# Kernel optimization log

Hardware: AMD Instinct MI355X
Metric: run time of the kernel (lower is better)

## Reference

```python
import jax, jax.numpy as jnp
import numpy as np

B, S, D, H, DFF = 4, 2048, 1024, 16, 4096
DK = D // H
EPS = 1e-5


def setup_inputs() -> dict:
    key = jax.random.key(0)
    ks = jax.random.split(key, 10)
    s = 0.02
    return {
        "x": jax.random.normal(ks[0], (B, S, D), jnp.float32),
        "wq": jax.random.normal(ks[1], (D, D), jnp.float32) * s,
        "wk": jax.random.normal(ks[2], (D, D), jnp.float32) * s,
        "wv": jax.random.normal(ks[3], (D, D), jnp.float32) * s,
        "wo": jax.random.normal(ks[4], (D, D), jnp.float32) * s,
        "w1": jax.random.normal(ks[5], (D, DFF), jnp.float32) * s,
        "b1": jnp.zeros((DFF,), jnp.float32),
        "w2": jax.random.normal(ks[6], (DFF, D), jnp.float32) * s,
        "b2": jnp.zeros((D,), jnp.float32),
        "g1": jnp.ones((D,), jnp.float32),
        "be1": jnp.zeros((D,), jnp.float32),
        "g2": jnp.ones((D,), jnp.float32),
        "be2": jnp.zeros((D,), jnp.float32),
    }


def _layernorm(x, g, b):
    mu = jnp.mean(x, axis=-1, keepdims=True)
    var = jnp.mean(jnp.square(x - mu), axis=-1, keepdims=True)
    return (x - mu) * jax.lax.rsqrt(var + EPS) * g + b


def reference(x, wq, wk, wv, wo, w1, b1, w2, b2, g1, be1, g2, be2):
    # --- self-attention block (pre-LN) ---
    residual = x
    h = _layernorm(x, g1, be1)
    q = (h @ wq).reshape(B, S, H, DK).transpose(0, 2, 1, 3)  # [B,H,S,DK]
    k = (h @ wk).reshape(B, S, H, DK).transpose(0, 2, 1, 3)
    v = (h @ wv).reshape(B, S, H, DK).transpose(0, 2, 1, 3)
    scores = jnp.einsum("bhqd,bhkd->bhqk", q, k) / jnp.sqrt(jnp.float32(DK))
    weights = jax.nn.softmax(scores, axis=-1)
    weights = jnp.nan_to_num(weights, nan=0.0)
    attn = jnp.einsum("bhqk,bhkd->bhqd", weights, v)
    attn = attn.transpose(0, 2, 1, 3).reshape(B, S, D)
    x = residual + attn @ wo
    # --- FFN block (pre-LN) ---
    residual = x
    h = _layernorm(x, g2, be2)
    h = jax.nn.relu(h @ w1 + b1) @ w2 + b2
    return residual + h
```

## Files before the change

kernel.cpp:

```cpp
#include <hip/hip_runtime.h>
#include <stdint.h>

#define B_ 4
#define S_ 2048
#define D_ 1024
#define H_ 16
#define DFF_ 4096
#define QSTR 3072

typedef __attribute__((ext_vector_type(8))) short short8;
typedef __attribute__((ext_vector_type(4))) short short4v;
typedef __attribute__((ext_vector_type(4))) float floatx4;
typedef __attribute__((ext_vector_type(16))) float floatx16;

typedef const __attribute__((address_space(1))) void* gas_ptr;
typedef __attribute__((address_space(3))) void* las_ptr;

__device__ __forceinline__ short f2bf(float f) {
  union { float f; uint32_t u; } v; v.f = f;
  uint32_t r = v.u + 0x7fffu + ((v.u >> 16) & 1u);
  return (short)(r >> 16);
}

__global__ __launch_bounds__(256) void ln_kernel(
    const float* __restrict__ x, const float* __restrict__ g,
    const float* __restrict__ be, short* __restrict__ out)
{
  const int row = blockIdx.x;
  const int tid = threadIdx.x;
  const float4 v = ((const float4*)(x + (size_t)row * D_))[tid];
  float s1 = v.x + v.y + v.z + v.w;
  float s2 = v.x*v.x + v.y*v.y + v.z*v.z + v.w*v.w;
#pragma unroll
  for (int off = 1; off < 64; off <<= 1) {
    s1 += __shfl_xor(s1, off);
    s2 += __shfl_xor(s2, off);
  }
  __shared__ float r1[4], r2[4];
  if ((tid & 63) == 0) { r1[tid >> 6] = s1; r2[tid >> 6] = s2; }
  __syncthreads();
  s1 = r1[0] + r1[1] + r1[2] + r1[3];
  s2 = r2[0] + r2[1] + r2[2] + r2[3];
  const float mu = s1 * (1.0f / D_);
  const float var = s2 * (1.0f / D_) - mu * mu;
  const float rs = rsqrtf(var + 1e-5f);
  const float4 gv = ((const float4*)g)[tid];
  const float4 bv = ((const float4*)be)[tid];
  short4v o;
  o.x = f2bf((v.x - mu) * rs * gv.x + bv.x);
  o.y = f2bf((v.y - mu) * rs * gv.y + bv.y);
  o.z = f2bf((v.z - mu) * rs * gv.z + bv.z);
  o.w = f2bf((v.w - mu) * rs * gv.w + bv.w);
  *(short4v*)&out[(size_t)row * D_ + tid * 4] = o;
}

__global__ __launch_bounds__(256) void transpose_all(
    const float* __restrict__ wq, const float* __restrict__ wk,
    const float* __restrict__ wv, const float* __restrict__ wo,
    const float* __restrict__ w1, const float* __restrict__ w2,
    short* __restrict__ wqkvT, short* __restrict__ woT,
    short* __restrict__ w1T, short* __restrict__ w2T)
{
  const uint32_t pid = blockIdx.x;
  const float* in; short* out;
  int R, C, tile, xsh;
  if (pid < 4096) {
    const int which = pid >> 10; tile = pid & 1023;
    R = 1024; C = 1024; xsh = 5;
    in  = (which == 0) ? wq : (which == 1) ? wk : (which == 2) ? wv : wo;
    out = (which == 3) ? woT : wqkvT + (size_t)which * 1024 * 1024;
  } else if (pid < 8192) {
    tile = pid - 4096; R = 1024; C = 4096; xsh = 7; in = w1; out = w1T;
  } else {
    tile = pid - 8192; R = 4096; C = 1024; xsh = 5; in = w2; out = w2T;
  }
  const int c0 = (tile & ((1 << xsh) - 1)) * 32;
  const int r0 = (tile >> xsh) * 32;

  __shared__ float t[32][33];
  const int tx = threadIdx.x & 31, ty = threadIdx.x >> 5;
#pragma unroll
  for (int i = 0; i < 4; i++)
    t[ty + i * 8][tx] = in[(size_t)(r0 + ty + i * 8) * C + c0 + tx];
  __syncthreads();
#pragma unroll
  for (int i = 0; i < 4; i++)
    out[(size_t)(c0 + ty + i * 8) * R + r0 + tx] = f2bf(t[tx][ty + i * 8]);
}

__global__ __launch_bounds__(256, 4) void gemm_bt(
    const short* __restrict__ A, const short* __restrict__ Bt,
    float* __restrict__ outf, short* __restrict__ outb,
    short* __restrict__ outbK, short* __restrict__ vtT,
    const float* __restrict__ bias, const float* __restrict__ resid,
    int M, int N, int K, int do_relu, int split, int group)
{
  __shared__ short As[2 * 128 * 32];
  __shared__ short Bs[2 * 128 * 32];
  const int tid = threadIdx.x;
  const int wave = tid >> 6;
  const int lane = tid & 63;
  const int quad = lane >> 4;
  const int l16 = lane & 15;

  const uint32_t nblk = gridDim.x;
  const uint32_t pid = blockIdx.y * nblk + blockIdx.x;
  const uint32_t nig = (uint32_t)group * nblk;
  const uint32_t gid = pid / nig;
  const uint32_t within = pid - gid * nig;
  const uint32_t bm = gid * group + within % group;
  const uint32_t bn = within / group;
  const int tm = bm * 128;
  const int tn = bn * 128;

  const int wm = (wave & 1) * 64;
  const int wn = (wave >> 1) * 64;
  const int srow = lane >> 2;
  const int scol = ((lane & 3) ^ ((lane >> 3) & 3)) * 8;
  const int rg = (l16 >> 1) & 3;

  floatx4 acc[4][4];
#pragma unroll
  for (int i = 0; i < 4; i++)
#pragma unroll
    for (int j = 0; j < 4; j++) acc[i][j] = floatx4{0.f, 0.f, 0.f, 0.f};

  const short* gA0 = A + (size_t)(tm + wave * 32 + srow) * K + scol;
  const short* gB0 = Bt + (size_t)(tn + wave * 32 + srow) * K + scol;

  for (int kt = 0; kt < K; kt += 64) {
    __syncthreads();
    __builtin_amdgcn_global_load_lds((gas_ptr)(gA0 + kt),                      (las_ptr)(&As[wave * 1024]),        16, 0, 0);
    __builtin_amdgcn_global_load_lds((gas_ptr)(gA0 + kt + (size_t)16 * K),     (las_ptr)(&As[wave * 1024 + 512]),  16, 0, 0);
    __builtin_amdgcn_global_load_lds((gas_ptr)(gB0 + kt),                      (las_ptr)(&Bs[wave * 1024]),        16, 0, 0);
    __builtin_amdgcn_global_load_lds((gas_ptr)(gB0 + kt + (size_t)16 * K),     (las_ptr)(&Bs[wave * 1024 + 512]),  16, 0, 0);
    __builtin_amdgcn_global_load_lds((gas_ptr)(gA0 + kt + 32),                 (las_ptr)(&As[4096 + wave * 1024]),       16, 0, 0);
    __builtin_amdgcn_global_load_lds((gas_ptr)(gA0 + kt + 32 + (size_t)16 * K),(las_ptr)(&As[4096 + wave * 1024 + 512]), 16, 0, 0);
    __builtin_amdgcn_global_load_lds((gas_ptr)(gB0 + kt + 32),                 (las_ptr)(&Bs[4096 + wave * 1024]),       16, 0, 0);
    __builtin_amdgcn_global_load_lds((gas_ptr)(gB0 + kt + 32 + (size_t)16 * K),(las_ptr)(&Bs[4096 + wave * 1024 + 512]), 16, 0, 0);
    __syncthreads();

#pragma unroll
    for (int ksub = 0; ksub < 2; ksub++) {
      const int hb = ksub * 4096;
      short8 af[4], bfv[4];
#pragma unroll
      for (int mi = 0; mi < 4; mi++)
        af[mi] = *(const short8*)&As[hb + (wm + mi * 16 + l16) * 32 + (quad ^ rg) * 8];
#pragma unroll
      for (int ni = 0; ni < 4; ni++)
        bfv[ni] = *(const short8*)&Bs[hb + (wn + ni * 16 + l16) * 32 + (quad ^ rg) * 8];
#pragma unroll
      for (int mi = 0; mi < 4; mi++)
#pragma unroll
        for (int ni = 0; ni < 4; ni++)
          acc[mi][ni] = __builtin_amdgcn_mfma_f32_16x16x32_bf16(af[mi], bfv[ni], acc[mi][ni], 0, 0, 0);
    }
  }

  short* ob = outb;
  int Nst = N;
  int cbase = tn;
  int vpart = 0;
  if (split) {
    const int part = tn >> 10;
    if (part == 2) vpart = 1;
    else ob = (part == 0) ? outb : outbK;
    Nst = D_;
    cbase = tn & (D_ - 1);
  }

  if (vpart) {
#pragma unroll
    for (int mi = 0; mi < 4; mi++) {
      const int row0 = tm + wm + mi * 16 + quad * 4;
      const int bb = row0 >> 11, s0r = row0 & 2047;
#pragma unroll
      for (int ni = 0; ni < 4; ni++) {
        const int cst = cbase + wn + ni * 16 + l16;
        short4v o;
#pragma unroll
        for (int r = 0; r < 4; r++) o[r] = f2bf(acc[mi][ni][r]);
        *(short4v*)&vtT[((size_t)(bb << 10) + cst) * (size_t)S_ + s0r] = o;
      }
    }
    return;
  }

#pragma unroll
  for (int mi = 0; mi < 4; mi++) {
    const int row0 = tm + wm + mi * 16 + quad * 4;
#pragma unroll
    for (int ni = 0; ni < 4; ni++) {
      const int col = tn + wn + ni * 16 + l16;
      const int cst = cbase + wn + ni * 16 + l16;
      const float bv = bias ? bias[col] : 0.0f;
#pragma unroll
      for (int r = 0; r < 4; r++) {
        const size_t idx = (size_t)(row0 + r) * Nst + cst;
        float v = acc[mi][ni][r] + bv;
        if (do_relu) v = fmaxf(v, 0.0f);
        if (resid) v += resid[idx];
        if (outf) outf[idx] = v;
        if (ob) ob[idx] = f2bf(v);
      }
    }
  }
}

__global__ __launch_bounds__(256, 4) void gemm_bt_n64(
    const short* __restrict__ A, const short* __restrict__ Bt,
    float* __restrict__ outf,
    const float* __restrict__ bias, const float* __restrict__ resid,
    int M, int N, int K, int group)
{
  __shared__ short As[2 * 128 * 32];
  __shared__ short Bs[2 * 64 * 32];
  const int tid = threadIdx.x;
  const int wave = tid >> 6;
  const int lane = tid & 63;
  const int quad = lane >> 4;
  const int l16 = lane & 15;

  const uint32_t nblk = gridDim.x;
  const uint32_t pid = blockIdx.y * nblk + blockIdx.x;
  const uint32_t nig = (uint32_t)group * nblk;
  const uint32_t gid = pid / nig;
  const uint32_t within = pid - gid * nig;
  const uint32_t bm = gid * group + within % group;
  const uint32_t bn = within / group;
  const int tm = bm * 128;
  const int tn = bn * 64;

  const int wm = (wave & 1) * 64;
  const int wn = (wave >> 1) * 32;
  const int srow = lane >> 2;
  const int scol = (lane & 3) * 8;

  floatx4 acc[4][2];
#pragma unroll
  for (int i = 0; i < 4; i++)
#pragma unroll
    for (int j = 0; j < 2; j++) acc[i][j] = floatx4{0.f, 0.f, 0.f, 0.f};

  const short* gA0 = A + (size_t)(tm + wave * 32 + srow) * K + scol;
  const short* gB0 = Bt + (size_t)(tn + wave * 16 + srow) * K + scol;

  for (int kt = 0; kt < K; kt += 64) {
    __syncthreads();
    __builtin_amdgcn_global_load_lds((gas_ptr)(gA0 + kt),                      (las_ptr)(&As[wave * 1024]),        16, 0, 0);
    __builtin_amdgcn_global_load_lds((gas_ptr)(gA0 + kt + (size_t)16 * K),     (las_ptr)(&As[wave * 1024 + 512]),  16, 0, 0);
    __builtin_amdgcn_global_load_lds((gas_ptr)(gA0 + kt + 32),                 (las_ptr)(&As[4096 + wave * 1024]),       16, 0, 0);
    __builtin_amdgcn_global_load_lds((gas_ptr)(gA0 + kt + 32 + (size_t)16 * K),(las_ptr)(&As[4096 + wave * 1024 + 512]), 16, 0, 0);
    __builtin_amdgcn_global_load_lds((gas_ptr)(gB0 + kt),      (las_ptr)(&Bs[wave * 512]),        16, 0, 0);
    __builtin_amdgcn_global_load_lds((gas_ptr)(gB0 + kt + 32), (las_ptr)(&Bs[2048 + wave * 512]), 16, 0, 0);
    __syncthreads();

#pragma unroll
    for (int ksub = 0; ksub < 2; ksub++) {
      const int ha = ksub * 4096;
      const int hbv = ksub * 2048;
      short8 af[4], bfv[2];
#pragma unroll
      for (int mi = 0; mi < 4; mi++)
        af[mi] = *(const short8*)&As[ha + (wm + mi * 16 + l16) * 32 + quad * 8];
#pragma unroll
      for (int ni = 0; ni < 2; ni++)
        bfv[ni] = *(const short8*)&Bs[hbv + (wn + ni * 16 + l16) * 32 + quad * 8];
#pragma unroll
      for (int mi = 0; mi < 4; mi++)
#pragma unroll
        for (int ni = 0; ni < 2; ni++)
          acc[mi][ni] = __builtin_amdgcn_mfma_f32_16x16x32_bf16(af[mi], bfv[ni], acc[mi][ni], 0, 0, 0);
    }
  }

#pragma unroll
  for (int mi = 0; mi < 4; mi++) {
    const int row0 = tm + wm + mi * 16 + quad * 4;
#pragma unroll
    for (int ni = 0; ni < 2; ni++) {
      const int col = tn + wn + ni * 16 + l16;
      const float bv = bias ? bias[col] : 0.0f;
#pragma unroll
      for (int r = 0; r < 4; r++) {
        const size_t idx = (size_t)(row0 + r) * N + col;
        float v = acc[mi][ni][r] + bv;
        if (resid) v += resid[idx];
        outf[idx] = v;
      }
    }
  }
}

__device__ __forceinline__ int swz64(int row) {
  return (row & 7) ^ ((row >> 3) & 3);
}
__device__ __forceinline__ int kvidx(int row, int scol) {
  return (row << 6) + (scol ^ (swz64(row) << 3));
}

__global__ __launch_bounds__(256, 4) void attn_kernel(
    const short* __restrict__ qb, const short* __restrict__ kb,
    const short* __restrict__ vtb, short* __restrict__ attb)
{
  __shared__ short Ks[2][64 * 64];
  __shared__ short Vts[2][64 * 64];
  __shared__ float lbuf[4][32];

  const int tid = threadIdx.x;
  const int wave = tid >> 6, lane = tid & 63;
  const int l31 = lane & 31, hi = lane >> 5;
  const int qt = blockIdx.x, bh = blockIdx.y;
  const int b = bh >> 4, h = bh & 15;
  const size_t rowbase = (size_t)b * S_;
  const int hcol = h * 64;

  const int lr = lane >> 3, lg = lane & 7;
  const int sgran = (lg ^ lr ^ wave) * 8;
  const short* ksrc = kb + (rowbase + wave * 8 + lr) * D_ + hcol + sgran;
  const short* vsrc = vtb + ((size_t)bh * 64 + wave * 8 + lr) * S_ + sgran;

  short8 qf[4];
  {
    const short* gq = qb + (rowbase + qt * 128 + wave * 32 + l31) * D_ + hcol + hi * 8;
#pragma unroll
    for (int st = 0; st < 4; st++) {
      short8 t = *(const short8*)(gq + st * 16);
#pragma unroll
      for (int i = 0; i < 8; i++) {
        const float f = __uint_as_float(((uint32_t)(uint16_t)t[i]) << 16) * 0.18033688f;
        t[i] = (short)((__float_as_uint(f) + 0x8000u) >> 16);
      }
      qf[st] = t;
    }
  }

  floatx16 Of[2];
#pragma unroll
  for (int nd = 0; nd < 2; nd++)
#pragma unroll
    for (int i = 0; i < 16; i++) Of[nd][i] = 0.f;
  float lrun0 = 0.f, lrun1 = 0.f;

  __builtin_amdgcn_global_load_lds((gas_ptr)ksrc,                      (las_ptr)(&Ks[0][(wave * 8) * 64]),        16, 0, 0);
  __builtin_amdgcn_global_load_lds((gas_ptr)(ksrc + (size_t)32 * D_),  (las_ptr)(&Ks[0][(32 + wave * 8) * 64]),   16, 0, 0);
  __builtin_amdgcn_global_load_lds((gas_ptr)vsrc,                      (las_ptr)(&Vts[0][(wave * 8) * 64]),       16, 0, 0);
  __builtin_amdgcn_global_load_lds((gas_ptr)(vsrc + (size_t)32 * S_),  (las_ptr)(&Vts[0][(32 + wave * 8) * 64]),  16, 0, 0);

  for (int kt = 0; kt < S_; kt += 64) {
    const int cur = (kt >> 6) & 1;
    __syncthreads();

    if (kt + 64 < S_) {
      const int nxt = cur ^ 1;
      const short* kp = ksrc + (size_t)(kt + 64) * D_;
      const short* vp = vsrc + (kt + 64);
      __builtin_amdgcn_global_load_lds((gas_ptr)kp,                      (las_ptr)(&Ks[nxt][(wave * 8) * 64]),        16, 0, 0);
      __builtin_amdgcn_global_load_lds((gas_ptr)(kp + (size_t)32 * D_),  (las_ptr)(&Ks[nxt][(32 + wave * 8) * 64]),   16, 0, 0);
      __builtin_amdgcn_global_load_lds((gas_ptr)vp,                      (las_ptr)(&Vts[nxt][(wave * 8) * 64]),       16, 0, 0);
      __builtin_amdgcn_global_load_lds((gas_ptr)(vp + (size_t)32 * S_),  (las_ptr)(&Vts[nxt][(32 + wave * 8) * 64]),  16, 0, 0);
    }

#pragma unroll
    for (int sub = 0; sub < 2; sub++) {
      floatx16 s;
#pragma unroll
      for (int i = 0; i < 16; i++) s[i] = 0.f;
      __builtin_amdgcn_s_setprio(1);
#pragma unroll
      for (int st = 0; st < 4; st++) {
        const short8 kf = *(const short8*)&Ks[cur][kvidx(sub * 32 + l31, st * 16 + hi * 8)];
        s = __builtin_amdgcn_mfma_f32_32x32x16_bf16(kf, qf[st], s, 0, 0, 0);
      }
      __builtin_amdgcn_s_setprio(0);
      float p[16];
#pragma unroll
      for (int i = 0; i < 16; i++) {
        p[i] = __builtin_amdgcn_exp2f(s[i]);
        if (i & 1) lrun1 += p[i]; else lrun0 += p[i];
      }
      short8 pf[2];
#pragma unroll
      for (int kw = 0; kw < 2; kw++) {
        const int o = kw * 8;
        uint32_t wa, wb, wc, wd;
        asm("v_cvt_pk_bf16_f32 %0, %1, %2" : "=v"(wa) : "v"(p[o + 0]), "v"(p[o + 1]));
        asm("v_cvt_pk_bf16_f32 %0, %1, %2" : "=v"(wb) : "v"(p[o + 4]), "v"(p[o + 5]));
        asm("v_cvt_pk_bf16_f32 %0, %1, %2" : "=v"(wc) : "v"(p[o + 2]), "v"(p[o + 3]));
        asm("v_cvt_pk_bf16_f32 %0, %1, %2" : "=v"(wd) : "v"(p[o + 6]), "v"(p[o + 7]));
        asm("v_permlane32_swap_b32 %0, %1" : "+v"(wa), "+v"(wb));
        asm("v_permlane32_swap_b32 %0, %1" : "+v"(wc), "+v"(wd));
        union { uint32_t u[4]; short8 s8; } pk;
        pk.u[0] = wa; pk.u[1] = wc; pk.u[2] = wb; pk.u[3] = wd;
        pf[kw] = pk.s8;
      }
      __builtin_amdgcn_s_setprio(1);
#pragma unroll
      for (int kw = 0; kw < 2; kw++)
#pragma unroll
        for (int nd = 0; nd < 2; nd++) {
          const short8 vf = *(const short8*)&Vts[cur][kvidx(nd * 32 + l31, sub * 32 + kw * 16 + hi * 8)];
          Of[nd] = __builtin_amdgcn_mfma_f32_32x32x16_bf16(pf[kw], vf, Of[nd], 0, 0, 0);
        }
      __builtin_amdgcn_s_setprio(0);
    }
  }

  const float lrun = lrun0 + lrun1;
  const float ltot = lrun + __shfl_xor(lrun, 32);
  if (hi == 0) lbuf[wave][l31] = ltot;
  asm volatile("" ::: "memory");
#pragma unroll
  for (int reg = 0; reg < 16; reg++) {
    const int q = (reg & 3) + 4 * hi + 8 * (reg >> 2);
    const float inv = 1.0f / lbuf[wave][q];
    const size_t base = (rowbase + qt * 128 + wave * 32 + q) * D_ + hcol + l31;
    attb[base]      = f2bf(Of[0][reg] * inv);
    attb[base + 32] = f2bf(Of[1][reg] * inv);
  }
}

extern "C" void kernel_launch(void* const* d_in, const int* in_sizes, int n_in,
                              void* d_out, int out_size, void* d_ws, size_t ws_size,
                              hipStream_t stream) {
  const float* x   = (const float*)d_in[0];
  const float* wq  = (const float*)d_in[1];
  const float* wk  = (const float*)d_in[2];
  const float* wv  = (const float*)d_in[3];
  const float* wo  = (const float*)d_in[4];
  const float* w1  = (const float*)d_in[5];
  const float* b1  = (const float*)d_in[6];
  const float* w2  = (const float*)d_in[7];
  const float* b2  = (const float*)d_in[8];
  const float* g1  = (const float*)d_in[9];
  const float* be1 = (const float*)d_in[10];
  const float* g2  = (const float*)d_in[11];
  const float* be2 = (const float*)d_in[12];
  float* out = (float*)d_out;

  const size_t MROWS = (size_t)B_ * S_;
  char* p = (char*)d_ws;
  auto take = [&](size_t bytes) { char* r = p; p += (bytes + 255) & ~(size_t)255; return r; };
  short* hb    = (short*)take(MROWS * D_ * 2);
  short* h2b   = (short*)take(MROWS * D_ * 2);
  short* qbuf  = (short*)take(MROWS * D_ * 2);
  short* kbuf  = (short*)take(MROWS * D_ * 2);
  short* vtb   = (short*)take(MROWS * D_ * 2);
  short* attb  = (short*)take(MROWS * D_ * 2);
  short* ffb   = (short*)take(MROWS * DFF_ * 2);
  short* wqkvT = (short*)take((size_t)3 * D_ * D_ * 2);
  short* woT   = (short*)take((size_t)D_ * D_ * 2);
  short* w1T   = (short*)take((size_t)D_ * DFF_ * 2);
  short* w2T   = (short*)take((size_t)DFF_ * D_ * 2);
  float* x1    = (float*)take(MROWS * D_ * 4);

  transpose_all<<<12288, 256, 0, stream>>>(wq, wk, wv, wo, w1, w2,
                                           wqkvT, woT, w1T, w2T);

  ln_kernel<<<MROWS, 256, 0, stream>>>(x, g1, be1, hb);

  gemm_bt<<<dim3(QSTR / 128, MROWS / 128), 256, 0, stream>>>(
      hb, wqkvT, nullptr, qbuf, kbuf, vtb, nullptr, nullptr, MROWS, QSTR, D_, 0, 1, 8);

  attn_kernel<<<dim3(S_ / 128, B_ * H_), 256, 0, stream>>>(qbuf, kbuf, vtb, attb);

  gemm_bt<<<dim3(D_ / 128, MROWS / 128), 256, 0, stream>>>(
      attb, woT, x1, nullptr, nullptr, nullptr, nullptr, x, MROWS, D_, D_, 0, 0, 8);

  ln_kernel<<<MROWS, 256, 0, stream>>>(x1, g2, be2, h2b);

  gemm_bt<<<dim3(DFF_ / 128, MROWS / 128), 256, 0, stream>>>(
      h2b, w1T, nullptr, ffb, nullptr, nullptr, b1, nullptr, MROWS, DFF_, D_, 1, 0, 8);

  gemm_bt<<<dim3(D_ / 128, MROWS / 128), 256, 0, stream>>>(
      ffb, w2T, out, nullptr, nullptr, nullptr, b2, x1, MROWS, D_, DFF_, 0, 0, 8);

  (void)in_sizes; (void)n_in; (void)out_size; (void)ws_size;
}
```

Measured before the change: 528.6 us.

## Double-buffer GEMM LDS tiles and prefetch next K-slice during MFMA compute

Restructures the main bf16 GEMM loop into a two-stage ping-pong pipeline. The tile for step k+1 is loaded asynchronously into the alternate LDS buffer while MFMAs run on the current one, with one barrier per 32-wide K step instead of two per 64-wide step. It also raises wave priority around the MFMA block and removes the unused-looking N=64 GEMM variant. This should hide global-to-LDS latency, at the cost of twice as many loop iterations and barriers. The visible code does not show whether the host still calls the removed N=64 kernel.

```diff
diff --git a/kernel.cpp b/kernel.cpp
--- a/kernel.cpp
+++ b/kernel.cpp
@@ -95,8 +95,8 @@
     const float* __restrict__ bias, const float* __restrict__ resid,
     int M, int N, int K, int do_relu, int split, int group)
 {
-  __shared__ short As[2 * 128 * 32];
-  __shared__ short Bs[2 * 128 * 32];
+  __shared__ short As[2][128 * 32];
+  __shared__ short Bs[2][128 * 32];
   const int tid = threadIdx.x;
   const int wave = tid >> 6;
   const int lane = tid & 63;
@@ -116,7 +116,7 @@
   const int wm = (wave & 1) * 64;
   const int wn = (wave >> 1) * 64;
   const int srow = lane >> 2;
-  const int scol = ((lane & 3) ^ ((lane >> 3) & 3)) * 8;
+  const int sgran = ((lane & 3) ^ ((lane >> 3) & 3)) * 8;
   const int rg = (l16 >> 1) & 3;
 
   floatx4 acc[4][4];
@@ -125,38 +125,41 @@
 #pragma unroll
     for (int j = 0; j < 4; j++) acc[i][j] = floatx4{0.f, 0.f, 0.f, 0.f};
 
-  const short* gA0 = A + (size_t)(tm + wave * 32 + srow) * K + scol;
-  const short* gB0 = Bt + (size_t)(tn + wave * 32 + srow) * K + scol;
-
-  for (int kt = 0; kt < K; kt += 64) {
+  const short* gA0 = A + (size_t)(tm + wave * 32 + srow) * K + sgran;
+  const short* gB0 = Bt + (size_t)(tn + wave * 32 + srow) * K + sgran;
+
+#define GB_STAGE(buf, kk)                                                                                   \
+  do {                                                                                                      \
+    __builtin_amdgcn_global_load_lds((gas_ptr)(gA0 + (kk)),                   (las_ptr)(&As[buf][wave * 1024]),       16, 0, 0); \
+    __builtin_amdgcn_global_load_lds((gas_ptr)(gA0 + (kk) + (size_t)16 * K),  (las_ptr)(&As[buf][wave * 1024 + 512]), 16, 0, 0); \
+    __builtin_amdgcn_global_load_lds((gas_ptr)(gB0 + (kk)),                   (las_ptr)(&Bs[buf][wave * 1024]),       16, 0, 0); \
+    __builtin_amdgcn_global_load_lds((gas_ptr)(gB0 + (kk) + (size_t)16 * K),  (las_ptr)(&Bs[buf][wave * 1024 + 512]), 16, 0, 0); \
+  } while (0)
+
+  GB_STAGE(0, 0);
+
+  for (int kt = 0; kt < K; kt += 32) {
+    const int cur = (kt >> 5) & 1;
     __syncthreads();
-    __builtin_amdgcn_global_load_lds((gas_ptr)(gA0 + kt),                      (las_ptr)(&As[wave * 1024]),        16, 0, 0);
-    __builtin_amdgcn_global_load_lds((gas_ptr)(gA0 + kt + (size_t)16 * K),     (las_ptr)(&As[wave * 1024 + 512]),  16, 0, 0);
-    __builtin_amdgcn_global_load_lds((gas_ptr)(gB0 + kt),                      (las_ptr)(&Bs[wave * 1024]),        16, 0, 0);
-    __builtin_amdgcn_global_load_lds((gas_ptr)(gB0 + kt + (size_t)16 * K),     (las_ptr)(&Bs[wave * 1024 + 512]),  16, 0, 0);
-    __builtin_amdgcn_global_load_lds((gas_ptr)(gA0 + kt + 32),                 (las_ptr)(&As[4096 + wave * 1024]),       16, 0, 0);
-    __builtin_amdgcn_global_load_lds((gas_ptr)(gA0 + kt + 32 + (size_t)16 * K),(las_ptr)(&As[4096 + wave * 1024 + 512]), 16, 0, 0);
-    __builtin_amdgcn_global_load_lds((gas_ptr)(gB0 + kt + 32),                 (las_ptr)(&Bs[4096 + wave * 1024]),       16, 0, 0);
-    __builtin_amdgcn_global_load_lds((gas_ptr)(gB0 + kt + 32 + (size_t)16 * K),(las_ptr)(&Bs[4096 + wave * 1024 + 512]), 16, 0, 0);
-    __syncthreads();
-
-#pragma unroll
-    for (int ksub = 0; ksub < 2; ksub++) {
-      const int hb = ksub * 4096;
-      short8 af[4], bfv[4];
-#pragma unroll
-      for (int mi = 0; mi < 4; mi++)
-        af[mi] = *(const short8*)&As[hb + (wm + mi * 16 + l16) * 32 + (quad ^ rg) * 8];
+
+    if (kt + 32 < K) GB_STAGE(cur ^ 1, kt + 32);
+
+    short8 af[4], bfv[4];
+#pragma unroll
+    for (int mi = 0; mi < 4; mi++)
+      af[mi] = *(const short8*)&As[cur][(wm + mi * 16 + l16) * 32 + (quad ^ rg) * 8];
+#pragma unroll
+    for (int ni = 0; ni < 4; ni++)
+      bfv[ni] = *(const short8*)&Bs[cur][(wn + ni * 16 + l16) * 32 + (quad ^ rg) * 8];
+    __builtin_amdgcn_s_setprio(1);
+#pragma unroll
+    for (int mi = 0; mi < 4; mi++)
 #pragma unroll
       for (int ni = 0; ni < 4; ni++)
-        bfv[ni] = *(const short8*)&Bs[hb + (wn + ni * 16 + l16) * 32 + (quad ^ rg) * 8];
-#pragma unroll
-      for (int mi = 0; mi < 4; mi++)
-#pragma unroll
-        for (int ni = 0; ni < 4; ni++)
-          acc[mi][ni] = __builtin_amdgcn_mfma_f32_16x16x32_bf16(af[mi], bfv[ni], acc[mi][ni], 0, 0, 0);
-    }
-  }
+        acc[mi][ni] = __builtin_amdgcn_mfma_f32_16x16x32_bf16(af[mi], bfv[ni], acc[mi][ni], 0, 0, 0);
+    __builtin_amdgcn_s_setprio(0);
+  }
+#undef GB_STAGE
 
   short* ob = outb;
   int Nst = N;
@@ -203,91 +206,6 @@
         if (resid) v += resid[idx];
         if (outf) outf[idx] = v;
         if (ob) ob[idx] = f2bf(v);
-      }
-    }
-  }
-}
-
-__global__ __launch_bounds__(256, 4) void gemm_bt_n64(
-    const short* __restrict__ A, const short* __restrict__ Bt,
-    float* __restrict__ outf,
-    const float* __restrict__ bias, const float* __restrict__ resid,
-    int M, int N, int K, int group)
-{
-  __shared__ short As[2 * 128 * 32];
-  __shared__ short Bs[2 * 64 * 32];
-  const int tid = threadIdx.x;
-  const int wave = tid >> 6;
-  const int lane = tid & 63;
-  const int quad = lane >> 4;
-  const int l16 = lane & 15;
-
-  const uint32_t nblk = gridDim.x;
-  const uint32_t pid = blockIdx.y * nblk + blockIdx.x;
-  const uint32_t nig = (uint32_t)group * nblk;
-  const uint32_t gid = pid / nig;
-  const uint32_t within = pid - gid * nig;
-  const uint32_t bm = gid * group + within % group;
-  const uint32_t bn = within / group;
-  const int tm = bm * 128;
-  const int tn = bn * 64;
-
-  const int wm = (wave & 1) * 64;
-  const int wn = (wave >> 1) * 32;
-  const int srow = lane >> 2;
-  const int scol = (lane & 3) * 8;
-
-  floatx4 acc[4][2];
-#pragma unroll
-  for (int i = 0; i < 4; i++)
-#pragma unroll
-    for (int j = 0; j < 2; j++) acc[i][j] = floatx4{0.f, 0.f, 0.f, 0.f};
-
-  const short* gA0 = A + (size_t)(tm + wave * 32 + srow) * K + scol;
-  const short* gB0 = Bt + (size_t)(tn + wave * 16 + srow) * K + scol;
-
-  for (int kt = 0; kt < K; kt += 64) {
-    __syncthreads();
-    __builtin_amdgcn_global_load_lds((gas_ptr)(gA0 + kt),                      (las_ptr)(&As[wave * 1024]),        16, 0, 0);
-    __builtin_amdgcn_global_load_lds((gas_ptr)(gA0 + kt + (size_t)16 * K),     (las_ptr)(&As[wave * 1024 + 512]),  16, 0, 0);
-    __builtin_amdgcn_global_load_lds((gas_ptr)(gA0 + kt + 32),                 (las_ptr)(&As[4096 + wave * 1024]),       16, 0, 0);
-    __builtin_amdgcn_global_load_lds((gas_ptr)(gA0 + kt + 32 + (size_t)16 * K),(las_ptr)(&As[4096 + wave * 1024 + 512]), 16, 0, 0);
-    __builtin_amdgcn_global_load_lds((gas_ptr)(gB0 + kt),      (las_ptr)(&Bs[wave * 512]),        16, 0, 0);
-    __builtin_amdgcn_global_load_lds((gas_ptr)(gB0 + kt + 32), (las_ptr)(&Bs[2048 + wave * 512]), 16, 0, 0);
-    __syncthreads();
-
-#pragma unroll
-    for (int ksub = 0; ksub < 2; ksub++) {
-      const int ha = ksub * 4096;
-      const int hbv = ksub * 2048;
-      short8 af[4], bfv[2];
-#pragma unroll
-      for (int mi = 0; mi < 4; mi++)
-        af[mi] = *(const short8*)&As[ha + (wm + mi * 16 + l16) * 32 + quad * 8];
-#pragma unroll
-      for (int ni = 0; ni < 2; ni++)
-        bfv[ni] = *(const short8*)&Bs[hbv + (wn + ni * 16 + l16) * 32 + quad * 8];
-#pragma unroll
-      for (int mi = 0; mi < 4; mi++)
-#pragma unroll
-        for (int ni = 0; ni < 2; ni++)
-          acc[mi][ni] = __builtin_amdgcn_mfma_f32_16x16x32_bf16(af[mi], bfv[ni], acc[mi][ni], 0, 0, 0);
-    }
-  }
-
-#pragma unroll
-  for (int mi = 0; mi < 4; mi++) {
-    const int row0 = tm + wm + mi * 16 + quad * 4;
-#pragma unroll
-    for (int ni = 0; ni < 2; ni++) {
-      const int col = tn + wn + ni * 16 + l16;
-      const float bv = bias ? bias[col] : 0.0f;
-#pragma unroll
-      for (int r = 0; r < 4; r++) {
-        const size_t idx = (size_t)(row0 + r) * N + col;
-        float v = acc[mi][ni][r] + bv;
-        if (resid) v += resid[idx];
-        outf[idx] = v;
       }
     }
   }
```

New measurement: 543.8 us. 2.9% more time.
